# Optimization experiments

Hardware: AMD Instinct MI355X
Metric: run time of the kernel (lower is better)

Reference implementation:

```python
import jax, jax.numpy as jnp
import numpy as np

BS, H = 2048, 1024
XDIM = 2048 + 4 * 64  # x + R*W = 2304
IN = XDIM + 2 * H     # 4352


def setup_inputs() -> dict:
    key = jax.random.key(0)
    ks = jax.random.split(key, 11)
    s = 1.0 / np.sqrt(IN)  # torch Linear default init scale
    return {
        "input_x": jax.random.normal(ks[0], (BS, XDIM), jnp.float32),
        "previous_time": jax.random.normal(ks[1], (BS, H), jnp.float32),
        "previous_layer": jax.random.normal(ks[2], (BS, H), jnp.float32),
        "old_state": jnp.zeros((BS, H), jnp.float32),
        "Wi": jax.random.normal(ks[3], (H, IN), jnp.float32) * s,
        "bi": jax.random.normal(ks[4], (H,), jnp.float32) * s,
        "Wf": jax.random.normal(ks[5], (H, IN), jnp.float32) * s,
        "bf": jax.random.normal(ks[6], (H,), jnp.float32) * s,
        "Wo": jax.random.normal(ks[7], (H, IN), jnp.float32) * s,
        "bo": jax.random.normal(ks[8], (H,), jnp.float32) * s,
        "Ws": jax.random.normal(ks[9], (H, IN), jnp.float32) * s,
        "bs_state": jax.random.normal(ks[10], (H,), jnp.float32) * s,
    }


def reference(input_x, previous_time, previous_layer, old_state,
              Wi, bi, Wf, bf, Wo, bo, Ws, bs_state):
    # semicolon_input: [bs, x + R*W + 2h]
    z = jnp.concatenate([input_x, previous_time, previous_layer], axis=1)
    # Fuse the four projections into one GEMM: [bs, 4h]
    W_all = jnp.concatenate([Wi, Wf, Wo, Ws], axis=0)          # [4h, IN]
    b_all = jnp.concatenate([bi, bf, bo, bs_state], axis=0)    # [4h]
    proj = z @ W_all.T + b_all
    gi, gf, go, gs = jnp.split(proj, 4, axis=1)
    input_gate = jax.nn.sigmoid(gi)
    forget_gate = jax.nn.sigmoid(gf)
    output_gate = jax.nn.sigmoid(go)
    new_state = forget_gate * old_state + input_gate * jnp.tanh(gs)
    new_hidden = output_gate * jnp.tanh(new_state)
    return new_hidden
```

## Files before the change

kernel.cpp:

```cpp
#include <hip/hip_runtime.h>
#include <stdint.h>
#include <stddef.h>

#define M_DIM 2048
#define N_DIM 4096
#define K_DIM 4352
#define H_DIM 1024
#define X_DIM 2304

#define A_OFF 0u
#define B_OFF 17825792u

typedef __bf16 bf16x8 __attribute__((ext_vector_type(8)));
typedef float f32x4 __attribute__((ext_vector_type(4)));

__device__ __forceinline__ unsigned short f32_to_bf16(float f) {
    unsigned u = __float_as_uint(f);
    u += 0x7FFFu + ((u >> 16) & 1u);
    return (unsigned short)(u >> 16);
}

__device__ __forceinline__ float sigm_(float x) { return 1.f / (1.f + __expf(-x)); }
__device__ __forceinline__ float tanh_(float x) {
    x = fminf(15.f, fmaxf(-15.f, x));
    float e = __expf(2.f * x);
    return (e - 1.f) / (e + 1.f);
}

__global__ __launch_bounds__(256) void convert_kernel(
    const float* __restrict__ x, const float* __restrict__ pt,
    const float* __restrict__ pl,
    const float* __restrict__ Wi, const float* __restrict__ Wf,
    const float* __restrict__ Wo, const float* __restrict__ Ws,
    unsigned short* __restrict__ Abf, unsigned short* __restrict__ Bbf)
{
    const int row = blockIdx.x;
    const float* srow = nullptr;
    unsigned short* drow;
    if (row < M_DIM) {
        drow = Abf + (size_t)row * K_DIM;
    } else {
        int n = row - M_DIM;
        int g = n >> 10, h = n & 1023;
        const float* W = (g == 0) ? Wi : (g == 1) ? Wf : (g == 2) ? Wo : Ws;
        srow = W + (size_t)h * K_DIM;
        drow = Bbf + (size_t)(h * 4 + g) * K_DIM;
    }

    for (int c8 = threadIdx.x; c8 < K_DIM / 8; c8 += 256) {
        int col = c8 * 8;
        const float* s;
        if (row < M_DIM) {
            if (col < X_DIM)              s = x  + (size_t)row * X_DIM + col;
            else if (col < X_DIM + H_DIM) s = pt + (size_t)row * H_DIM + (col - X_DIM);
            else                          s = pl + (size_t)row * H_DIM + (col - X_DIM - H_DIM);
        } else {
            s = srow + col;
        }
        float4 v0 = ((const float4*)s)[0];
        float4 v1 = ((const float4*)s)[1];
        union { unsigned short h[8]; uint4 u; } r;
        r.h[0] = f32_to_bf16(v0.x); r.h[1] = f32_to_bf16(v0.y);
        r.h[2] = f32_to_bf16(v0.z); r.h[3] = f32_to_bf16(v0.w);
        r.h[4] = f32_to_bf16(v1.x); r.h[5] = f32_to_bf16(v1.y);
        r.h[6] = f32_to_bf16(v1.z); r.h[7] = f32_to_bf16(v1.w);
        *(uint4*)(drow + col) = r.u;
    }
}

__global__ __launch_bounds__(512, 2) void gemm_fused(
    const unsigned short* __restrict__ A,
    const unsigned short* __restrict__ B,
    const float* __restrict__ old_state,
    const float* __restrict__ bi, const float* __restrict__ bfv,
    const float* __restrict__ bo, const float* __restrict__ bs,
    float* __restrict__ out)
{
    __shared__ __align__(16) char smem[98304];
    float* sP = (float*)smem;

    const int tid  = threadIdx.x;
    const int lane = tid & 63;
    const int wave = tid >> 6;
    const int wm = (wave >> 2) * 64;
    const int wn = (wave & 3) * 64;

    const int b   = blockIdx.x;
    const int xcd = b & 7;
    const int j   = b >> 3;
    const int m0  = (j >> 1) * 128;
    const int n0  = (xcd * 2 + (j & 1)) * 256;

    const int srow_ = tid >> 2;
    const int kb_   = (tid & 3) ^ ((tid >> 3) & 3);
    const unsigned short* Asrc  = A + (size_t)(m0 + srow_)       * K_DIM + kb_ * 8;
    const unsigned short* Bsrc0 = B + (size_t)(n0 + srow_)       * K_DIM + kb_ * 8;
    const unsigned short* Bsrc1 = B + (size_t)(n0 + 128 + srow_) * K_DIM + kb_ * 8;

    const int fr  = lane & 15;
    const int kb0 = lane >> 4;
    const int swz = (kb0 ^ ((fr >> 1) & 3)) * 16;
    const int aoff = (wm + fr) * 64 + swz;
    const int boff = 8192 + (wn + fr) * 64 + swz;

    f32x4 acc[4][4];
#pragma unroll
    for (int i = 0; i < 4; ++i)
#pragma unroll
        for (int jj = 0; jj < 4; ++jj) acc[i][jj] = (f32x4){0.f, 0.f, 0.f, 0.f};

    auto stage = [&](int h, int c) {
        const size_t koff = (size_t)h * 32;
        __builtin_amdgcn_global_load_lds(
            (const __attribute__((address_space(1))) unsigned*)(Asrc + koff),
            (__attribute__((address_space(3))) unsigned*)(smem + c * 24576 + wave * 1024),
            16, 0, 0);
        __builtin_amdgcn_global_load_lds(
            (const __attribute__((address_space(1))) unsigned*)(Bsrc0 + koff),
            (__attribute__((address_space(3))) unsigned*)(smem + c * 24576 + 8192 + wave * 1024),
            16, 0, 0);
        __builtin_amdgcn_global_load_lds(
            (const __attribute__((address_space(1))) unsigned*)(Bsrc1 + koff),
            (__attribute__((address_space(3))) unsigned*)(smem + c * 24576 + 16384 + wave * 1024),
            16, 0, 0);
    };

    bf16x8 a0[4], b0[4], a1[4], b1[4];

#define VM3 asm volatile("s_waitcnt vmcnt(3)" ::: "memory")
#define VM0 asm volatile("s_waitcnt vmcnt(0)" ::: "memory")
#define VMNONE ((void)0)

#define READS(AN, BN, NBUF)                                                     \
    _Pragma("unroll")                                                           \
    for (int i_ = 0; i_ < 4; ++i_) {                                            \
        AN[i_] = *(const bf16x8*)(smem + (NBUF) * 24576 + aoff + i_ * 1024);    \
        BN[i_] = *(const bf16x8*)(smem + (NBUF) * 24576 + boff + i_ * 1024);    \
    }

#define MFMAS(AC, BC)                                                           \
    __builtin_amdgcn_s_setprio(1);                                              \
    _Pragma("unroll")                                                           \
    for (int i_ = 0; i_ < 4; ++i_)                                              \
        _Pragma("unroll")                                                       \
        for (int j_ = 0; j_ < 4; ++j_)                                          \
            acc[i_][j_] = __builtin_amdgcn_mfma_f32_16x16x32_bf16(              \
                AC[i_], BC[j_], acc[i_][j_], 0, 0, 0);                          \
    __builtin_amdgcn_s_setprio(0);

#define PHASE(AC, BC, AN, BN, NBUF, SH, DOSTAGE, VMLINE, DOBAR)                 \
    do {                                                                        \
        READS(AN, BN, NBUF);                                                    \
        if (DOSTAGE) stage((SH), (SH) & 3);                                     \
        __builtin_amdgcn_sched_barrier(0);                                      \
        MFMAS(AC, BC);                                                          \
        __builtin_amdgcn_sched_barrier(0);                                      \
        VMLINE;                                                                 \
        if (DOBAR) __builtin_amdgcn_s_barrier();                                \
    } while (0)

    stage(0, 0); stage(1, 1); stage(2, 2);
    VM3;
    __builtin_amdgcn_s_barrier();
    READS(a0, b0, 0);

    for (int p4 = 0; p4 < 132; p4 += 4) {
        PHASE(a0, b0, a1, b1, 1, p4 + 3, true, VM3, true);
        PHASE(a1, b1, a0, b0, 2, p4 + 4, true, VM3, true);
        PHASE(a0, b0, a1, b1, 3, p4 + 5, true, VM3, true);
        PHASE(a1, b1, a0, b0, 0, p4 + 6, true, VM3, true);
    }
    PHASE(a0, b0, a1, b1, 1, 135, true,  VM3,    true);
    PHASE(a1, b1, a0, b0, 2, 0,   false, VM0,    true);
    PHASE(a0, b0, a1, b1, 3, 0,   false, VMNONE, false);
    MFMAS(a1, b1);

#undef PHASE
#undef READS
#undef MFMAS
#undef VM3
#undef VM0
#undef VMNONE

    const int cw = lane & 15;
    const int rw = (lane >> 4) * 4;
    const int hl = tid & 15;
    const int rb = tid >> 4;

    for (int p = 0; p < 4; ++p) {
        __syncthreads();
        if ((wave & 3) == p) {
#pragma unroll
            for (int i = 0; i < 4; ++i)
#pragma unroll
                for (int jj = 0; jj < 4; ++jj)
#pragma unroll
                    for (int r = 0; r < 4; ++r)
                        sP[(wm + i * 16 + rw + r) * 76 + jj * 16 + cw] = acc[i][jj][r];
        }
        __syncthreads();

        const int hg = (n0 >> 2) + p * 16 + hl;
        const float b_i = bi[hg], b_f = bfv[hg], b_o = bo[hg], b_s = bs[hg];
#pragma unroll
        for (int k = 0; k < 4; ++k) {
            const int row = rb + 32 * k;
            float4 g = *(const float4*)(sP + row * 76 + hl * 4);
            const size_t oidx = (size_t)(m0 + row) * H_DIM + hg;
            float old = old_state[oidx];
            float ig = sigm_(g.x + b_i);
            float fg = sigm_(g.y + b_f);
            float og = sigm_(g.z + b_o);
            float ts = tanh_(g.w + b_s);
            out[oidx] = og * tanh_(fg * old + ig * ts);
        }
    }
}

extern "C" void kernel_launch(void* const* d_in, const int* in_sizes, int n_in,
                              void* d_out, int out_size, void* d_ws, size_t ws_size,
                              hipStream_t stream) {
    const float* x   = (const float*)d_in[0];
    const float* pt  = (const float*)d_in[1];
    const float* pl  = (const float*)d_in[2];
    const float* old = (const float*)d_in[3];
    const float* Wi  = (const float*)d_in[4];
    const float* bi  = (const float*)d_in[5];
    const float* Wf  = (const float*)d_in[6];
    const float* bf  = (const float*)d_in[7];
    const float* Wo  = (const float*)d_in[8];
    const float* bo  = (const float*)d_in[9];
    const float* Ws  = (const float*)d_in[10];
    const float* bs  = (const float*)d_in[11];
    float* out = (float*)d_out;

    char* ws = (char*)d_ws;
    unsigned short* Abf = (unsigned short*)(ws + A_OFF);
    unsigned short* Bbf = (unsigned short*)(ws + B_OFF);

    convert_kernel<<<M_DIM + N_DIM, 256, 0, stream>>>(x, pt, pl, Wi, Wf, Wo, Ws, Abf, Bbf);

    gemm_fused<<<256, 512, 0, stream>>>(Abf, Bbf, old, bi, bf, bo, bs, out);
}
```

Baseline: 233.0 us.

## Switch GEMM to 256x128 tiles with 4 waves each computing 128x64

```diff
diff --git a/kernel.cpp b/kernel.cpp
--- a/kernel.cpp
+++ b/kernel.cpp
@@ -68,7 +68,7 @@
     }
 }
 
-__global__ __launch_bounds__(512, 2) void gemm_fused(
+__global__ __launch_bounds__(256, 1) void gemm_fused(
     const unsigned short* __restrict__ A,
     const unsigned short* __restrict__ B,
     const float* __restrict__ old_state,
@@ -82,71 +82,69 @@
     const int tid  = threadIdx.x;
     const int lane = tid & 63;
     const int wave = tid >> 6;
-    const int wm = (wave >> 2) * 64;
-    const int wn = (wave & 3) * 64;
+    const int wm = (wave >> 1) * 128;
+    const int wn = (wave & 1) * 64;
 
     const int b   = blockIdx.x;
     const int xcd = b & 7;
     const int j   = b >> 3;
-    const int m0  = (j >> 1) * 128;
-    const int n0  = (xcd * 2 + (j & 1)) * 256;
-
-    const int srow_ = tid >> 2;
-    const int kb_   = (tid & 3) ^ ((tid >> 3) & 3);
-    const unsigned short* Asrc  = A + (size_t)(m0 + srow_)       * K_DIM + kb_ * 8;
-    const unsigned short* Bsrc0 = B + (size_t)(n0 + srow_)       * K_DIM + kb_ * 8;
-    const unsigned short* Bsrc1 = B + (size_t)(n0 + 128 + srow_) * K_DIM + kb_ * 8;
+    const int m0  = (j >> 2) * 256;
+    const int n0  = (xcd * 4 + (j & 3)) * 128;
+
+    const int urow = tid >> 2;
+    const int ukb  = (tid & 3) ^ ((tid >> 3) & 3);
+    const unsigned short* Asrc = A + (size_t)(m0 + urow) * K_DIM + ukb * 8;
+    const unsigned short* Bsrc = B + (size_t)(n0 + urow) * K_DIM + ukb * 8;
 
     const int fr  = lane & 15;
     const int kb0 = lane >> 4;
     const int swz = (kb0 ^ ((fr >> 1) & 3)) * 16;
     const int aoff = (wm + fr) * 64 + swz;
-    const int boff = 8192 + (wn + fr) * 64 + swz;
-
-    f32x4 acc[4][4];
-#pragma unroll
-    for (int i = 0; i < 4; ++i)
+    const int boff = 16384 + (wn + fr) * 64 + swz;
+
+    f32x4 acc[8][4];
+#pragma unroll
+    for (int i = 0; i < 8; ++i)
 #pragma unroll
         for (int jj = 0; jj < 4; ++jj) acc[i][jj] = (f32x4){0.f, 0.f, 0.f, 0.f};
 
     auto stage = [&](int h, int c) {
         const size_t koff = (size_t)h * 32;
-        __builtin_amdgcn_global_load_lds(
-            (const __attribute__((address_space(1))) unsigned*)(Asrc + koff),
-            (__attribute__((address_space(3))) unsigned*)(smem + c * 24576 + wave * 1024),
-            16, 0, 0);
-        __builtin_amdgcn_global_load_lds(
-            (const __attribute__((address_space(1))) unsigned*)(Bsrc0 + koff),
-            (__attribute__((address_space(3))) unsigned*)(smem + c * 24576 + 8192 + wave * 1024),
-            16, 0, 0);
-        __builtin_amdgcn_global_load_lds(
-            (const __attribute__((address_space(1))) unsigned*)(Bsrc1 + koff),
-            (__attribute__((address_space(3))) unsigned*)(smem + c * 24576 + 16384 + wave * 1024),
-            16, 0, 0);
+#pragma unroll
+        for (int i = 0; i < 4; ++i)
+            __builtin_amdgcn_global_load_lds(
+                (const __attribute__((address_space(1))) unsigned*)(Asrc + (size_t)i * 64 * K_DIM + koff),
+                (__attribute__((address_space(3))) unsigned*)(smem + c * 24576 + i * 4096 + wave * 1024),
+                16, 0, 0);
+#pragma unroll
+        for (int i = 0; i < 2; ++i)
+            __builtin_amdgcn_global_load_lds(
+                (const __attribute__((address_space(1))) unsigned*)(Bsrc + (size_t)i * 64 * K_DIM + koff),
+                (__attribute__((address_space(3))) unsigned*)(smem + c * 24576 + 16384 + i * 4096 + wave * 1024),
+                16, 0, 0);
     };
 
-    bf16x8 a0[4], b0[4], a1[4], b1[4];
-
-#define VM3 asm volatile("s_waitcnt vmcnt(3)" ::: "memory")
-#define VM0 asm volatile("s_waitcnt vmcnt(0)" ::: "memory")
+    bf16x8 aA[8], bA[4], aB[8], bB[4];
+
+#define VM6  asm volatile("s_waitcnt vmcnt(6)"  ::: "memory")
+#define VM0  asm volatile("s_waitcnt vmcnt(0)"  ::: "memory")
 #define VMNONE ((void)0)
 
 #define READS(AN, BN, NBUF)                                                     \
     _Pragma("unroll")                                                           \
-    for (int i_ = 0; i_ < 4; ++i_) {                                            \
+    for (int i_ = 0; i_ < 8; ++i_)                                              \
         AN[i_] = *(const bf16x8*)(smem + (NBUF) * 24576 + aoff + i_ * 1024);    \
-        BN[i_] = *(const bf16x8*)(smem + (NBUF) * 24576 + boff + i_ * 1024);    \
-    }
+    _Pragma("unroll")                                                           \
+    for (int j_ = 0; j_ < 4; ++j_)                                              \
+        BN[j_] = *(const bf16x8*)(smem + (NBUF) * 24576 + boff + j_ * 1024);
 
 #define MFMAS(AC, BC)                                                           \
-    __builtin_amdgcn_s_setprio(1);                                              \
     _Pragma("unroll")                                                           \
-    for (int i_ = 0; i_ < 4; ++i_)                                              \
+    for (int i_ = 0; i_ < 8; ++i_)                                              \
         _Pragma("unroll")                                                       \
         for (int j_ = 0; j_ < 4; ++j_)                                          \
             acc[i_][j_] = __builtin_amdgcn_mfma_f32_16x16x32_bf16(              \
-                AC[i_], BC[j_], acc[i_][j_], 0, 0, 0);                          \
-    __builtin_amdgcn_s_setprio(0);
+                AC[i_], BC[j_], acc[i_][j_], 0, 0, 0);
 
 #define PHASE(AC, BC, AN, BN, NBUF, SH, DOSTAGE, VMLINE, DOBAR)                 \
     do {                                                                        \
@@ -160,25 +158,25 @@
     } while (0)
 
     stage(0, 0); stage(1, 1); stage(2, 2);
-    VM3;
+    VM6;
     __builtin_amdgcn_s_barrier();
-    READS(a0, b0, 0);
+    READS(aA, bA, 0);
 
     for (int p4 = 0; p4 < 132; p4 += 4) {
-        PHASE(a0, b0, a1, b1, 1, p4 + 3, true, VM3, true);
-        PHASE(a1, b1, a0, b0, 2, p4 + 4, true, VM3, true);
-        PHASE(a0, b0, a1, b1, 3, p4 + 5, true, VM3, true);
-        PHASE(a1, b1, a0, b0, 0, p4 + 6, true, VM3, true);
-    }
-    PHASE(a0, b0, a1, b1, 1, 135, true,  VM3,    true);
-    PHASE(a1, b1, a0, b0, 2, 0,   false, VM0,    true);
-    PHASE(a0, b0, a1, b1, 3, 0,   false, VMNONE, false);
-    MFMAS(a1, b1);
+        PHASE(aA, bA, aB, bB, 1, p4 + 3, true, VM6, true);
+        PHASE(aB, bB, aA, bA, 2, p4 + 4, true, VM6, true);
+        PHASE(aA, bA, aB, bB, 3, p4 + 5, true, VM6, true);
+        PHASE(aB, bB, aA, bA, 0, p4 + 6, true, VM6, true);
+    }
+    PHASE(aA, bA, aB, bB, 1, 135, true,  VM6,    true);
+    PHASE(aB, bB, aA, bA, 2, 0,   false, VM0,    true);
+    PHASE(aA, bA, aB, bB, 3, 0,   false, VMNONE, false);
+    MFMAS(aB, bB);
 
 #undef PHASE
 #undef READS
 #undef MFMAS
-#undef VM3
+#undef VM6
 #undef VM0
 #undef VMNONE
 
@@ -187,25 +185,25 @@
     const int hl = tid & 15;
     const int rb = tid >> 4;
 
-    for (int p = 0; p < 4; ++p) {
+    for (int p = 0; p < 2; ++p) {
         __syncthreads();
-        if ((wave & 3) == p) {
-#pragma unroll
-            for (int i = 0; i < 4; ++i)
+        if ((wave & 1) == p) {
+#pragma unroll
+            for (int i = 0; i < 8; ++i)
 #pragma unroll
                 for (int jj = 0; jj < 4; ++jj)
 #pragma unroll
                     for (int r = 0; r < 4; ++r)
-                        sP[(wm + i * 16 + rw + r) * 76 + jj * 16 + cw] = acc[i][jj][r];
+                        sP[(wm + i * 16 + rw + r) * 68 + jj * 16 + cw] = acc[i][jj][r];
         }
         __syncthreads();
 
         const int hg = (n0 >> 2) + p * 16 + hl;
         const float b_i = bi[hg], b_f = bfv[hg], b_o = bo[hg], b_s = bs[hg];
 #pragma unroll
-        for (int k = 0; k < 4; ++k) {
-            const int row = rb + 32 * k;
-            float4 g = *(const float4*)(sP + row * 76 + hl * 4);
+        for (int k = 0; k < 16; ++k) {
+            const int row = rb + 16 * k;
+            float4 g = *(const float4*)(sP + row * 68 + hl * 4);
             const size_t oidx = (size_t)(m0 + row) * H_DIM + hg;
             float old = old_state[oidx];
             float ig = sigm_(g.x + b_i);
@@ -240,5 +238,5 @@
 
     convert_kernel<<<M_DIM + N_DIM, 256, 0, stream>>>(x, pt, pl, Wi, Wf, Wo, Ws, Abf, Bbf);
 
-    gemm_fused<<<256, 512, 0, stream>>>(Abf, Bbf, old, bi, bf, bo, bs, out);
-}
+    gemm_fused<<<256, 256, 0, stream>>>(Abf, Bbf, old, bi, bf, bo, bs, out);
+}
```

New measurement: 241.8 us. 1.04x slower.
